# Optimization experiments

Hardware: AMD Instinct MI355X
Metric: run time of the kernel (lower is better)

## Reference

```python
import jax, jax.numpy as jnp
import numpy as np

N_NODES = 100000
N_EDGES = 1600000
IN_FEATS = 3
HID = 150
OUT = 64


def setup_inputs() -> dict:
    key = jax.random.key(0)
    ks = jax.random.split(key, 8)
    return {
        "x": jax.random.normal(ks[0], (N_NODES, IN_FEATS), dtype=jnp.float32),
        "src": jax.random.randint(ks[1], (N_EDGES,), 0, N_NODES, dtype=jnp.int32),
        "dst": jax.random.randint(ks[2], (N_EDGES,), 0, N_NODES, dtype=jnp.int32),
        "W1_self": jax.random.normal(ks[3], (IN_FEATS, HID), dtype=jnp.float32) / np.sqrt(IN_FEATS),
        "W1_neigh": jax.random.normal(ks[4], (IN_FEATS, HID), dtype=jnp.float32) / np.sqrt(IN_FEATS),
        "b1": jnp.zeros((HID,), dtype=jnp.float32),
        "W2_self": jax.random.normal(ks[5], (HID, OUT), dtype=jnp.float32) / np.sqrt(HID),
        "W2_neigh": jax.random.normal(ks[6], (HID, OUT), dtype=jnp.float32) / np.sqrt(HID),
        "b2": jnp.zeros((OUT,), dtype=jnp.float32),
    }


def _sage_conv(x, src, dst, W_self, W_neigh, b, n_nodes):
    # gather source features along edges, mean-reduce onto destinations
    msg = x[src]  # [E, F]
    agg = jax.ops.segment_sum(msg, dst, num_segments=n_nodes)  # [N, F]
    deg = jax.ops.segment_sum(jnp.ones((src.shape[0],), dtype=x.dtype), dst,
                              num_segments=n_nodes)
    h_neigh = agg / jnp.maximum(deg, 1.0)[:, None]
    return x @ W_self + h_neigh @ W_neigh + b


def reference(x, src, dst, W1_self, W1_neigh, b1, W2_self, W2_neigh, b2):
    n = x.shape[0]
    h = _sage_conv(x, src, dst, W1_self, W1_neigh, b1, n)
    h = jax.nn.relu(h)
    return _sage_conv(h, src, dst, W2_self, W2_neigh, b2, n)
```

## Files before the change

kernel.cpp:

```cpp
#include <hip/hip_runtime.h>

#define N_NODES 100000
#define N_PAD 100032
#define N_EDGES 1600000
#define HID 150
#define KPAD 160
#define HROW 168
#define OUTF 64
#define BSH 9
#define BUKN 512
#define NBUK ((N_NODES + BUKN - 1) / BUKN)
#define CAP 10240
#define TILE 4096
#define NTILE ((N_EDGES + TILE - 1) / TILE)
#define W1B_N (10 * 64 * 8)
#define W2T_N (128 * KPAD)

typedef short bf16x8 __attribute__((ext_vector_type(8)));
typedef float f32x4 __attribute__((ext_vector_type(4)));

__device__ __forceinline__ unsigned short f2bf(float f) {
    union { float f; unsigned u; } v; v.f = f;
    unsigned r = (v.u + 0x7FFFu + ((v.u >> 16) & 1u)) >> 16;
    return (unsigned short)r;
}

__device__ __forceinline__ float bf2f(unsigned short b) {
    union { unsigned u; float f; } v;
    v.u = ((unsigned)b) << 16;
    return v.f;
}

__global__ __launch_bounds__(256) void k_init0(int* __restrict__ bukcnt) {
    int tid = threadIdx.x;
    if (tid < NBUK) bukcnt[tid] = 0;
}

__global__ __launch_bounds__(256) void k_part(const float* __restrict__ x,
                                              float4* __restrict__ x4,
                                              const int* __restrict__ src,
                                              const int* __restrict__ dst,
                                              int* __restrict__ bukcnt,
                                              unsigned int* __restrict__ pairbuf,
                                              const float* __restrict__ W1s,
                                              const float* __restrict__ W1n,
                                              const float* __restrict__ b1,
                                              const float* __restrict__ W2s,
                                              const float* __restrict__ W2n,
                                              unsigned short* __restrict__ W1B,
                                              unsigned short* __restrict__ W2T) {
    __shared__ int cnt[NBUK];
    __shared__ int gbase[NBUK];
    int tid = threadIdx.x;
    int idx = blockIdx.x * 256 + tid;

    if (idx < W1B_N) {
        int t = idx >> 9;
        int r = idx & 511;
        int ln = r >> 3;
        int j = r & 7;
        int q = ln >> 4;
        int c = t * 16 + (ln & 15);
        float v = 0.0f;
        if (q == 0 && c < HID) {
            if (j < 3)       v = W1s[j * HID + c];
            else if (j == 3) v = b1[c];
            else if (j < 7)  v = W1n[(j - 4) * HID + c];
        }
        W1B[idx] = f2bf(v);
    } else if (idx < W1B_N + W2T_N) {
        int i2 = idx - W1B_N;
        int c = i2 / KPAD, k = i2 - c * KPAD;
        float v = 0.0f;
        if (k < HID) v = (c < 64) ? W2s[k * 64 + c] : W2n[k * 64 + (c - 64)];
        W2T[i2] = f2bf(v);
    }

    if (idx < N_NODES)
        x4[idx] = make_float4(x[idx * 3 + 0], x[idx * 3 + 1], x[idx * 3 + 2], 0.0f);

    int e0 = blockIdx.x * TILE;
    int n = min(TILE, N_EDGES - e0);

    for (int i = tid; i < NBUK; i += 256) cnt[i] = 0;
    __syncthreads();

    int myb[16];
    int mypos[16];
    unsigned int myv[16];
    #pragma unroll
    for (int j = 0; j < 16; ++j) {
        int ei = tid + j * 256;
        myb[j] = -1;
        if (ei < n) {
            int s = src[e0 + ei];
            int d = dst[e0 + ei];
            int b = d >> BSH;
            myb[j] = b;
            myv[j] = ((unsigned int)(d & (BUKN - 1)) << 17) | (unsigned int)s;
            mypos[j] = atomicAdd(&cnt[b], 1);
        }
    }
    __syncthreads();

    if (tid < NBUK) {
        int c = cnt[tid];
        gbase[tid] = c ? (tid * CAP + atomicAdd(&bukcnt[tid], c)) : 0;
    }
    __syncthreads();

    #pragma unroll
    for (int j = 0; j < 16; ++j) {
        if (myb[j] >= 0)
            pairbuf[gbase[myb[j]] + mypos[j]] = myv[j];
    }
}

__global__ __launch_bounds__(512) void k_fine(const int* __restrict__ bukcnt,
                                              const unsigned int* __restrict__ pairbuf,
                                              int2* __restrict__ rows,
                                              float* __restrict__ invd,
                                              int* __restrict__ csr_src) {
    __shared__ int deg[BUKN];
    __shared__ int sc[BUKN];
    int tid = threadIdx.x;
    int b = blockIdx.x;
    int n0 = b << BSH;
    int lo = b * CAP;
    int hi = lo + bukcnt[b];

    deg[tid] = 0;
    __syncthreads();
    for (int i = lo + tid; i < hi; i += 512)
        atomicAdd(&deg[pairbuf[i] >> 17], 1);
    __syncthreads();

    int d = deg[tid];
    sc[tid] = d;
    __syncthreads();
    for (int o = 1; o < 512; o <<= 1) {
        int a = sc[tid];
        int ap = (tid >= o) ? sc[tid - o] : 0;
        __syncthreads();
        sc[tid] = a + ap;
        __syncthreads();
    }
    int r = lo + sc[tid] - d;
    int node = n0 + tid;
    if (node < N_NODES) {
        rows[node] = make_int2(r, r + d);
        invd[node] = 1.0f / fmaxf((float)d, 1.0f);
    }
    __syncthreads();
    deg[tid] = r;
    __syncthreads();
    for (int i = lo + tid; i < hi; i += 512) {
        unsigned int v = pairbuf[i];
        int dl = v >> 17;
        int ofs = atomicAdd(&deg[dl], 1);
        csr_src[ofs] = (int)(v & 0x1FFFF);
    }
}

__global__ __launch_bounds__(256, 2) void k_gemm(
        const float4* __restrict__ x4,
        const int2* __restrict__ rows,
        const int* __restrict__ csr_src,
        const float* __restrict__ invd,
        const unsigned short* __restrict__ W1B,
        const unsigned short* __restrict__ W2T,
        const float* __restrict__ b2,
        unsigned short* __restrict__ ob) {
    __shared__ unsigned short shH[64 * HROW];
    const int n0 = blockIdx.x * 64;
    const int tid = threadIdx.x;
    const int lane = tid & 63;
    const int w = tid >> 6;
    const int c16 = lane & 15;
    const int quad = lane >> 4;
    const int nb = w * 16;

    float s0 = 0.f, s1 = 0.f, s2 = 0.f;
    {
        int j = lane >> 2;
        int sub = lane & 3;
        int nj = n0 + nb + j;
        if (nj < N_NODES) {
            int2 re = rows[nj];
            for (int i = re.x + sub; i < re.y; i += 4) {
                float4 v = x4[csr_src[i]];
                s0 += v.x; s1 += v.y; s2 += v.z;
            }
        }
        s0 += __shfl_xor(s0, 1, 64); s0 += __shfl_xor(s0, 2, 64);
        s1 += __shfl_xor(s1, 1, 64); s1 += __shfl_xor(s1, 2, 64);
        s2 += __shfl_xor(s2, 1, 64); s2 += __shfl_xor(s2, 2, 64);
        float id = (nj < N_NODES) ? invd[nj] : 0.0f;
        s0 *= id; s1 *= id; s2 *= id;
    }
    float xn0 = __shfl(s0, c16 * 4, 64);
    float xn1 = __shfl(s1, c16 * 4, 64);
    float xn2 = __shfl(s2, c16 * 4, 64);

    bf16x8 a8 = (bf16x8){0, 0, 0, 0, 0, 0, 0, 0};
    if (quad == 0) {
        int node = n0 + nb + c16;
        float4 xs = make_float4(0.f, 0.f, 0.f, 0.f);
        if (node < N_NODES) xs = x4[node];
        union { unsigned int u[4]; bf16x8 v; } t;
        t.u[0] = (unsigned int)f2bf(xs.x) | ((unsigned int)f2bf(xs.y) << 16);
        t.u[1] = (unsigned int)f2bf(xs.z) | (0x3F80u << 16);
        t.u[2] = (unsigned int)f2bf(xn0) | ((unsigned int)f2bf(xn1) << 16);
        t.u[3] = (unsigned int)f2bf(xn2);
        a8 = t.v;
    }

    #pragma unroll
    for (int t10 = 0; t10 < 10; ++t10) {
        bf16x8 b = *(const bf16x8*)&W1B[(t10 * 64 + lane) * 8];
        f32x4 z = __builtin_amdgcn_mfma_f32_16x16x32_bf16(
                      a8, b, (f32x4){0.f, 0.f, 0.f, 0.f}, 0, 0, 0);
        #pragma unroll
        for (int i = 0; i < 4; ++i) {
            float h = fmaxf(z[i], 0.0f);
            shH[(nb + quad * 4 + i) * HROW + t10 * 16 + c16] = f2bf(h);
        }
    }

    const int ko = quad * 8;
    f32x4 acc[8];
    #pragma unroll
    for (int t = 0; t < 8; ++t) acc[t] = (f32x4){0.f, 0.f, 0.f, 0.f};

    #pragma unroll
    for (int ks = 0; ks < 5; ++ks) {
        int k0 = ks * 32;
        bf16x8 a = *(const bf16x8*)&shH[(nb + c16) * HROW + k0 + ko];
        #pragma unroll
        for (int t = 0; t < 8; ++t) {
            bf16x8 b = *(const bf16x8*)&W2T[(t * 16 + c16) * KPAD + k0 + ko];
            acc[t] = __builtin_amdgcn_mfma_f32_16x16x32_bf16(a, b, acc[t], 0, 0, 0);
        }
    }

    const int rbase = n0 + nb + quad * 4;
    #pragma unroll
    for (int t = 0; t < 8; ++t) {
        int cc = t * 16 + c16;
        float badd = (t < 4) ? b2[cc] : 0.0f;
        #pragma unroll
        for (int i = 0; i < 4; ++i) {
            int node = rbase + i;
            if (node < N_NODES) ob[(size_t)node * 128 + cc] = f2bf(acc[t][i] + badd);
        }
    }
}

__global__ __launch_bounds__(256) void k_pull(const int2* __restrict__ rows,
                                              const int* __restrict__ csr_src,
                                              const unsigned short* __restrict__ ob,
                                              const float* __restrict__ invd,
                                              float* __restrict__ out) {
    int wid = blockIdx.x * 4 + (threadIdx.x >> 6);
    int lane = threadIdx.x & 63;
    int g = lane >> 3;
    int t = lane & 7;
    int n = wid * 8 + g;
    if (n >= N_NODES) return;
    int2 re = rows[n];

    float acc[8];
    #pragma unroll
    for (int q = 0; q < 8; ++q) acc[q] = 0.0f;

    #pragma unroll 4
    for (int i = re.x; i < re.y; ++i) {
        int s = csr_src[i];
        bf16x8 v = *(const bf16x8*)&ob[(size_t)s * 128 + 64 + t * 8];
        #pragma unroll
        for (int q = 0; q < 8; ++q) acc[q] += bf2f((unsigned short)v[q]);
    }

    float id = invd[n];
    bf16x8 sv = *(const bf16x8*)&ob[(size_t)n * 128 + t * 8];
    f32x4 o0, o1;
    o0[0] = bf2f((unsigned short)sv[0]) + acc[0] * id;
    o0[1] = bf2f((unsigned short)sv[1]) + acc[1] * id;
    o0[2] = bf2f((unsigned short)sv[2]) + acc[2] * id;
    o0[3] = bf2f((unsigned short)sv[3]) + acc[3] * id;
    o1[0] = bf2f((unsigned short)sv[4]) + acc[4] * id;
    o1[1] = bf2f((unsigned short)sv[5]) + acc[5] * id;
    o1[2] = bf2f((unsigned short)sv[6]) + acc[6] * id;
    o1[3] = bf2f((unsigned short)sv[7]) + acc[7] * id;
    *(f32x4*)&out[(size_t)n * OUTF + t * 8]     = o0;
    *(f32x4*)&out[(size_t)n * OUTF + t * 8 + 4] = o1;
}


static inline size_t al256(size_t v) { return (v + 255) & ~(size_t)255; }

extern "C" void kernel_launch(void* const* d_in, const int* in_sizes, int n_in,
                              void* d_out, int out_size, void* d_ws, size_t ws_size,
                              hipStream_t stream) {
    const float* x   = (const float*)d_in[0];
    const int*   src = (const int*)d_in[1];
    const int*   dst = (const int*)d_in[2];
    const float* W1s = (const float*)d_in[3];
    const float* W1n = (const float*)d_in[4];
    const float* b1  = (const float*)d_in[5];
    const float* W2s = (const float*)d_in[6];
    const float* W2n = (const float*)d_in[7];
    const float* b2  = (const float*)d_in[8];
    float* out = (float*)d_out;

    char* ws = (char*)d_ws;
    size_t off = 0;
    int2*  rows      = (int2*)(ws + off); off += al256((size_t)N_NODES * 8);
    int*   csr_src   = (int*)(ws + off); off += al256((size_t)NBUK * CAP * 4);
    float* invd      = (float*)(ws + off); off += al256((size_t)N_NODES * 4);
    unsigned short* ob = (unsigned short*)(ws + off); off += al256((size_t)N_NODES * 128 * 2);
    float4* x4       = (float4*)(ws + off); off += al256((size_t)N_NODES * 16);
    unsigned int* pairbuf = (unsigned int*)(ws + off); off += al256((size_t)NBUK * CAP * 4);
    int*   bukcnt    = (int*)(ws + off); off += al256((size_t)NBUK * 4);
    unsigned short* W1B = (unsigned short*)(ws + off); off += al256((size_t)W1B_N * 2);
    unsigned short* W2T = (unsigned short*)(ws + off); off += al256((size_t)W2T_N * 2);

    k_init0<<<1, 256, 0, stream>>>(bukcnt);
    k_part<<<NTILE, 256, 0, stream>>>(x, x4, src, dst, bukcnt, pairbuf,
                                      W1s, W1n, b1, W2s, W2n, W1B, W2T);
    k_fine<<<NBUK, 512, 0, stream>>>(bukcnt, pairbuf, rows, invd, csr_src);
    {
        int blocks = N_PAD / 64;
        k_gemm<<<blocks, 256, 0, stream>>>(x4, rows, csr_src, invd, W1B, W2T, b2, ob);
    }
    {
        int blocks = (N_NODES + 31) / 32;
        k_pull<<<blocks, 256, 0, stream>>>(rows, csr_src, ob, invd, out);
    }
}
```

Measured before the change: 115.8 us.

## Split each 16-node GEMM tile across two waves with 32-node blocks

The fused layer-1/layer-2 GEMM kernel now handles 32 nodes per block instead of 64. Each 16-node tile is shared by two waves that split the layer-1 output columns, the layer-2 output column tiles, and the neighbour gather (8 lanes per node instead of 4). Per-wave MFMA work and accumulator registers are halved and twice as many blocks launch, which should raise parallelism and latency hiding for the gather-heavy phase. In exchange it adds shared-memory exchange of neighbour means and two block-wide barriers.

Result: faster. 112.6 us (median of 2 runs) (-2.7%).

```diff
diff --git a/kernel.cpp b/kernel.cpp
--- a/kernel.cpp
+++ b/kernel.cpp
@@ -171,42 +171,51 @@
         const unsigned short* __restrict__ W2T,
         const float* __restrict__ b2,
         unsigned short* __restrict__ ob) {
-    __shared__ unsigned short shH[64 * HROW];
-    const int n0 = blockIdx.x * 64;
+    __shared__ unsigned short shH[32 * HROW];
+    __shared__ float shXN[32][3];
+    const int blk_n0 = blockIdx.x * 32;
     const int tid = threadIdx.x;
     const int lane = tid & 63;
     const int w = tid >> 6;
+    const int tile = w >> 1;
+    const int h = w & 1;
     const int c16 = lane & 15;
     const int quad = lane >> 4;
-    const int nb = w * 16;
-
-    float s0 = 0.f, s1 = 0.f, s2 = 0.f;
+    const int tn0 = tile * 16;
+
     {
-        int j = lane >> 2;
-        int sub = lane & 3;
-        int nj = n0 + nb + j;
+        int j = lane >> 3;
+        int sub = lane & 7;
+        int nj = blk_n0 + tn0 + h * 8 + j;
+        float s0 = 0.f, s1 = 0.f, s2 = 0.f;
         if (nj < N_NODES) {
             int2 re = rows[nj];
-            for (int i = re.x + sub; i < re.y; i += 4) {
+            for (int i = re.x + sub; i < re.y; i += 8) {
                 float4 v = x4[csr_src[i]];
                 s0 += v.x; s1 += v.y; s2 += v.z;
             }
         }
-        s0 += __shfl_xor(s0, 1, 64); s0 += __shfl_xor(s0, 2, 64);
-        s1 += __shfl_xor(s1, 1, 64); s1 += __shfl_xor(s1, 2, 64);
-        s2 += __shfl_xor(s2, 1, 64); s2 += __shfl_xor(s2, 2, 64);
-        float id = (nj < N_NODES) ? invd[nj] : 0.0f;
-        s0 *= id; s1 *= id; s2 *= id;
-    }
-    float xn0 = __shfl(s0, c16 * 4, 64);
-    float xn1 = __shfl(s1, c16 * 4, 64);
-    float xn2 = __shfl(s2, c16 * 4, 64);
+        s0 += __shfl_xor(s0, 1, 64); s0 += __shfl_xor(s0, 2, 64); s0 += __shfl_xor(s0, 4, 64);
+        s1 += __shfl_xor(s1, 1, 64); s1 += __shfl_xor(s1, 2, 64); s1 += __shfl_xor(s1, 4, 64);
+        s2 += __shfl_xor(s2, 1, 64); s2 += __shfl_xor(s2, 2, 64); s2 += __shfl_xor(s2, 4, 64);
+        if (sub == 0) {
+            float id = (nj < N_NODES) ? invd[nj] : 0.0f;
+            int rloc = tn0 + h * 8 + j;
+            shXN[rloc][0] = s0 * id;
+            shXN[rloc][1] = s1 * id;
+            shXN[rloc][2] = s2 * id;
+        }
+    }
+    __syncthreads();
 
     bf16x8 a8 = (bf16x8){0, 0, 0, 0, 0, 0, 0, 0};
     if (quad == 0) {
-        int node = n0 + nb + c16;
+        int node = blk_n0 + tn0 + c16;
         float4 xs = make_float4(0.f, 0.f, 0.f, 0.f);
         if (node < N_NODES) xs = x4[node];
+        float xn0 = shXN[tn0 + c16][0];
+        float xn1 = shXN[tn0 + c16][1];
+        float xn2 = shXN[tn0 + c16][2];
         union { unsigned int u[4]; bf16x8 v; } t;
         t.u[0] = (unsigned int)f2bf(xs.x) | ((unsigned int)f2bf(xs.y) << 16);
         t.u[1] = (unsigned int)f2bf(xs.z) | (0x3F80u << 16);
@@ -216,42 +225,45 @@
     }
 
     #pragma unroll
-    for (int t10 = 0; t10 < 10; ++t10) {
+    for (int m = 0; m < 5; ++m) {
+        int t10 = h * 5 + m;
         bf16x8 b = *(const bf16x8*)&W1B[(t10 * 64 + lane) * 8];
         f32x4 z = __builtin_amdgcn_mfma_f32_16x16x32_bf16(
                       a8, b, (f32x4){0.f, 0.f, 0.f, 0.f}, 0, 0, 0);
         #pragma unroll
         for (int i = 0; i < 4; ++i) {
-            float h = fmaxf(z[i], 0.0f);
-            shH[(nb + quad * 4 + i) * HROW + t10 * 16 + c16] = f2bf(h);
-        }
-    }
+            float hh = fmaxf(z[i], 0.0f);
+            shH[(tn0 + quad * 4 + i) * HROW + t10 * 16 + c16] = f2bf(hh);
+        }
+    }
+    __syncthreads();
 
     const int ko = quad * 8;
-    f32x4 acc[8];
-    #pragma unroll
-    for (int t = 0; t < 8; ++t) acc[t] = (f32x4){0.f, 0.f, 0.f, 0.f};
+    f32x4 acc[4];
+    #pragma unroll
+    for (int t = 0; t < 4; ++t) acc[t] = (f32x4){0.f, 0.f, 0.f, 0.f};
 
     #pragma unroll
     for (int ks = 0; ks < 5; ++ks) {
         int k0 = ks * 32;
-        bf16x8 a = *(const bf16x8*)&shH[(nb + c16) * HROW + k0 + ko];
+        bf16x8 a = *(const bf16x8*)&shH[(tn0 + c16) * HROW + k0 + ko];
         #pragma unroll
-        for (int t = 0; t < 8; ++t) {
+        for (int tt = 0; tt < 4; ++tt) {
+            int t = h * 4 + tt;
             bf16x8 b = *(const bf16x8*)&W2T[(t * 16 + c16) * KPAD + k0 + ko];
-            acc[t] = __builtin_amdgcn_mfma_f32_16x16x32_bf16(a, b, acc[t], 0, 0, 0);
-        }
-    }
-
-    const int rbase = n0 + nb + quad * 4;
-    #pragma unroll
-    for (int t = 0; t < 8; ++t) {
-        int cc = t * 16 + c16;
-        float badd = (t < 4) ? b2[cc] : 0.0f;
+            acc[tt] = __builtin_amdgcn_mfma_f32_16x16x32_bf16(a, b, acc[tt], 0, 0, 0);
+        }
+    }
+
+    const int rbase = blk_n0 + tn0 + quad * 4;
+    #pragma unroll
+    for (int tt = 0; tt < 4; ++tt) {
+        int cc = (h * 4 + tt) * 16 + c16;
+        float badd = (h == 0) ? b2[cc] : 0.0f;
         #pragma unroll
         for (int i = 0; i < 4; ++i) {
             int node = rbase + i;
-            if (node < N_NODES) ob[(size_t)node * 128 + cc] = f2bf(acc[t][i] + badd);
+            if (node < N_NODES) ob[(size_t)node * 128 + cc] = f2bf(acc[tt][i] + badd);
         }
     }
 }
@@ -330,7 +342,7 @@
                                       W1s, W1n, b1, W2s, W2n, W1B, W2T);
     k_fine<<<NBUK, 512, 0, stream>>>(bukcnt, pairbuf, rows, invd, csr_src);
     {
-        int blocks = N_PAD / 64;
+        int blocks = N_PAD / 32;
         k_gemm<<<blocks, 256, 0, stream>>>(x4, rows, csr_src, invd, W1B, W2T, b2, ob);
     }
     {
```
